# Kernel tuning notes

Hardware: AMD Instinct MI355X
Metric: run time of the kernel (lower is better)

## Reference

```python
import jax, jax.numpy as jnp
import numpy as np

NUM_CAPSULE = 32
DIM_CAPSULE = 16
NUM_ITERATIONS = 3


def squash(v):
    # v: [B, O, F]; squash along last dim
    norm = jnp.linalg.norm(v, axis=-1, keepdims=True)
    mag = norm * norm
    return v / norm * mag / (1.0 + mag)


def setup_inputs() -> dict:
    key = jax.random.key(0)
    k1, k2 = jax.random.split(key)
    B, L, H = 128, 512, 256
    O, F = NUM_CAPSULE, DIM_CAPSULE
    x = jax.random.normal(k1, (B, L, H), dtype=jnp.float32)
    # xavier_normal for [1, H, O*F]: std = sqrt(2 / (H + O*F))
    std = float(np.sqrt(2.0 / (H + O * F)))
    W = jax.random.normal(k2, (1, H, O * F), dtype=jnp.float32) * std
    return {"x": x, "W": W}


def reference(x, W):
    B, I, H = x.shape
    O, F = NUM_CAPSULE, DIM_CAPSULE
    # u: [B, I, O*F] -> [B, O, I, F]
    u = jnp.matmul(x, W)  # broadcasts shared W [1,H,O*F]
    u = u.reshape(B, I, O, F).transpose(0, 2, 1, 3)
    b = jnp.zeros((B, O, I), dtype=u.dtype)
    v = None
    for _ in range(NUM_ITERATIONS):
        c = jax.nn.softmax(b, axis=1)            # softmax over output capsules O
        v = jnp.einsum('boi,boif->bof', c, u)    # weighted aggregation
        v = squash(v)
        b = jnp.einsum('bof,boif->boi', v, u)    # agreement logits
    return v
```

## Files before the change

kernel.cpp:

```cpp
#include <hip/hip_runtime.h>

#define BB 128
#define II 512
#define HH 256
#define OO 32
#define FF 16
#define OF 512
#define CI 64
#define NP 8
#define CSTR 72

typedef __attribute__((ext_vector_type(8))) short short8;
typedef __attribute__((ext_vector_type(4))) float floatx4;

__device__ __forceinline__ ushort f2bf(float f) {
  unsigned u = __float_as_uint(f);
  u += 0x7FFFu + ((u >> 16) & 1u);
  return (ushort)(u >> 16);
}
__device__ __forceinline__ float bf2f(ushort u) {
  return __uint_as_float(((unsigned)u) << 16);
}
__device__ __forceinline__ int swzrow(int i) {
  return (i & 7) ^ (((i >> 3) & 3) << 1);
}

__global__ __launch_bounds__(256) void k_prep(
    const float* __restrict__ x, ushort* __restrict__ x16,
    float* __restrict__ xsum_part) {
  __shared__ float4 red[4][64];
  int t = threadIdx.x;
  int blk = blockIdx.x;
  int c4 = t & 63, grp = t >> 6;
  const float* xg = x + (size_t)blk * CI * HH;
  ushort* x16g = x16 + (size_t)blk * CI * HH;
  int g = c4 >> 1, s4 = (c4 & 1) * 4;
  float4 sum = make_float4(0.f, 0.f, 0.f, 0.f);
#pragma unroll
  for (int j = 0; j < 16; ++j) {
    int row = j * 4 + grp;
    float4 v4 = *(const float4*)(xg + (size_t)row * HH + c4 * 4);
    sum.x += v4.x; sum.y += v4.y; sum.z += v4.z; sum.w += v4.w;
    ushort4 u;
    u.x = f2bf(v4.x); u.y = f2bf(v4.y); u.z = f2bf(v4.z); u.w = f2bf(v4.w);
    *(ushort4*)&x16g[row * HH + (((g ^ swzrow(row)) << 3) + s4)] = u;
  }
  red[grp][c4] = sum;
  __syncthreads();
  if (t < 64) {
    float4 s = red[0][t];
    float4 s1 = red[1][t], s2 = red[2][t], s3 = red[3][t];
    s.x += s1.x + s2.x + s3.x; s.y += s1.y + s2.y + s3.y;
    s.z += s1.z + s2.z + s3.z; s.w += s1.w + s2.w + s3.w;
    *(float4*)&xsum_part[(size_t)blk * HH + t * 4] = s;
  }
}

__global__ __launch_bounds__(256) void k_v1(
    const float* __restrict__ xsum_part, const float* __restrict__ W,
    ushort* __restrict__ wvT16) {
  __shared__ float cxs[HH];
  __shared__ float red[4][16];
  __shared__ float vres[FF];
  int t = threadIdx.x;
  int blk = blockIdx.x;
  int b = blk >> 5, o = blk & 31;
  {
    const float* cp = xsum_part + (size_t)b * NP * HH + t;
    float a = 0.f;
#pragma unroll
    for (int p = 0; p < NP; ++p) a += cp[(size_t)p * HH];
    cxs[t] = a * (1.0f / 32.0f);
  }
  __syncthreads();
  int f = t & 15, hq = t >> 4;
  const float* wp = W + (size_t)hq * 16 * OF + o * FF + f;
  float acc = 0.f;
#pragma unroll
  for (int j = 0; j < 16; ++j)
    acc += cxs[hq * 16 + j] * wp[(size_t)j * OF];
  acc += __shfl_xor(acc, 16);
  acc += __shfl_xor(acc, 32);
  if ((t & 63) < 16) red[t >> 6][f] = acc;
  __syncthreads();
  if (t < 16) {
    float a = red[0][t] + red[1][t] + red[2][t] + red[3][t];
    float n2 = a * a;
#pragma unroll
    for (int mask = 1; mask < 16; mask <<= 1) n2 += __shfl_xor(n2, mask);
    float scale = sqrtf(n2) / (1.f + n2);
    vres[t] = a * scale;
  }
  __syncthreads();
  const float4* wq = (const float4*)(W + (size_t)t * OF + o * FF);
  const float4* vp = (const float4*)vres;
  float a = 0.f;
#pragma unroll
  for (int q = 0; q < 4; ++q) {
    float4 w4 = wq[q], v4 = vp[q];
    a += w4.x * v4.x + w4.y * v4.y + w4.z * v4.z + w4.w * v4.w;
  }
  wvT16[((size_t)b * OO + o) * HH + t] = f2bf(a);
}

__global__ __launch_bounds__(256, 4) void k_route(
    const ushort* __restrict__ x16, const ushort* __restrict__ wvT16,
    ushort* __restrict__ cxp16) {
  __shared__ alignas(16) ushort xs[CI * HH];
  __shared__ alignas(16) ushort c2[OO * CSTR];
  int t = threadIdx.x;
  int blk = blockIdx.x;
  int b = blk >> 3;
  int lane = t & 63, w = t >> 6;
  int l16 = lane & 15, quad = lane >> 4;

  const ushort* gt = x16 + (size_t)blk * (CI * HH);
#pragma unroll
  for (int it = 0; it < 8; ++it) {
    int off = (it * 4 + w) * 512;
    __builtin_amdgcn_global_load_lds(
        (const __attribute__((address_space(1))) unsigned*)(gt + off + lane * 8),
        (__attribute__((address_space(3))) unsigned*)(&xs[off]), 16, 0, 0);
  }
  asm volatile("s_waitcnt vmcnt(0)" ::: "memory");
  __syncthreads();

  int i_a = w * 16 + l16;
  int swa = swzrow(i_a);
  const ushort* xrow = &xs[i_a * HH];
  const ushort* wv0 = wvT16 + ((size_t)b * OO + l16) * HH + quad * 8;
  const ushort* wv1 = wv0 + 16 * HH;
  floatx4 acc0 = {0.f, 0.f, 0.f, 0.f}, acc1 = {0.f, 0.f, 0.f, 0.f};
#pragma unroll
  for (int ks = 0; ks < 8; ++ks) {
    short8 af = *(const short8*)(xrow + (((ks * 4 + quad) ^ swa) << 3));
    short8 b0 = *(const short8*)(wv0 + ks * 32);
    short8 b1 = *(const short8*)(wv1 + ks * 32);
    acc0 = __builtin_amdgcn_mfma_f32_16x16x32_bf16(af, b0, acc0, 0, 0, 0);
    acc1 = __builtin_amdgcn_mfma_f32_16x16x32_bf16(af, b1, acc1, 0, 0, 0);
  }
#pragma unroll
  for (int r = 0; r < 4; ++r) {
    float a0 = acc0[r], a1 = acc1[r];
    float m = fmaxf(a0, a1);
#pragma unroll
    for (int mask = 1; mask < 16; mask <<= 1) m = fmaxf(m, __shfl_xor(m, mask));
    float e0 = __expf(a0 - m), e1 = __expf(a1 - m);
    float s = e0 + e1;
#pragma unroll
    for (int mask = 1; mask < 16; mask <<= 1) s += __shfl_xor(s, mask);
    float inv = 1.f / s;
    int il = w * 16 + quad * 4 + r;
    c2[l16 * CSTR + il] = f2bf(e0 * inv);
    c2[(16 + l16) * CSTR + il] = f2bf(e1 * inv);
  }
  __syncthreads();

  short8 caf[2][2];
#pragma unroll
  for (int mt = 0; mt < 2; ++mt)
#pragma unroll
    for (int ks = 0; ks < 2; ++ks)
      caf[mt][ks] = *(const short8*)&c2[(mt * 16 + l16) * CSTR + ks * 32 + quad * 8];
  ushort* outp0 = cxp16 + (size_t)blk * OO * HH;
#pragma unroll
  for (int hi = 0; hi < 4; ++hi) {
    int ht = w * 4 + hi;
    int hh = ht * 16 + l16;
    int gq = hh >> 3, sub = hh & 7;
    floatx4 d0 = {0.f, 0.f, 0.f, 0.f}, d1 = {0.f, 0.f, 0.f, 0.f};
#pragma unroll
    for (int ks = 0; ks < 2; ++ks) {
      short8 bf;
#pragma unroll
      for (int e = 0; e < 8; ++e) {
        int i = ks * 32 + quad * 8 + e;
        bf[e] = (short)xs[i * HH + (((gq ^ e ^ (quad << 1)) << 3) + sub)];
      }
      d0 = __builtin_amdgcn_mfma_f32_16x16x32_bf16(caf[0][ks], bf, d0, 0, 0, 0);
      d1 = __builtin_amdgcn_mfma_f32_16x16x32_bf16(caf[1][ks], bf, d1, 0, 0, 0);
    }
    ushort* outp = outp0 + ht * 16 + l16;
#pragma unroll
    for (int r = 0; r < 4; ++r) {
      outp[(size_t)(quad * 4 + r) * HH] = f2bf(d0[r]);
      outp[(size_t)(16 + quad * 4 + r) * HH] = f2bf(d1[r]);
    }
  }
}

__global__ __launch_bounds__(256) void k_v2(
    const ushort* __restrict__ cxp16, const float* __restrict__ W,
    ushort* __restrict__ wvT16, float* __restrict__ out, int final_) {
  __shared__ float cxs[HH];
  __shared__ float red[4][16];
  __shared__ float vres[FF];
  int t = threadIdx.x;
  int blk = blockIdx.x;
  int b = blk >> 5, o = blk & 31;
  {
    const ushort* cp = cxp16 + (((size_t)b * NP) * OO + o) * HH + t;
    float a = 0.f;
#pragma unroll
    for (int p = 0; p < NP; ++p) a += bf2f(cp[(size_t)p * OO * HH]);
    cxs[t] = a;
  }
  __syncthreads();
  int f = t & 15, hq = t >> 4;
  const float* wp = W + (size_t)hq * 16 * OF + o * FF + f;
  float acc = 0.f;
#pragma unroll
  for (int j = 0; j < 16; ++j)
    acc += cxs[hq * 16 + j] * wp[(size_t)j * OF];
  acc += __shfl_xor(acc, 16);
  acc += __shfl_xor(acc, 32);
  if ((t & 63) < 16) red[t >> 6][f] = acc;
  __syncthreads();
  if (t < 16) {
    float a = red[0][t] + red[1][t] + red[2][t] + red[3][t];
    float n2 = a * a;
#pragma unroll
    for (int mask = 1; mask < 16; mask <<= 1) n2 += __shfl_xor(n2, mask);
    float scale = sqrtf(n2) / (1.f + n2);
    float res = a * scale;
    if (final_) out[(size_t)blk * FF + t] = res;
    else vres[t] = res;
  }
  if (!final_) {
    __syncthreads();
    const float4* wq = (const float4*)(W + (size_t)t * OF + o * FF);
    const float4* vp = (const float4*)vres;
    float a = 0.f;
#pragma unroll
    for (int q = 0; q < 4; ++q) {
      float4 w4 = wq[q], v4 = vp[q];
      a += w4.x * v4.x + w4.y * v4.y + w4.z * v4.z + w4.w * v4.w;
    }
    wvT16[((size_t)b * OO + o) * HH + t] = f2bf(a);
  }
}

extern "C" void kernel_launch(void* const* d_in, const int* in_sizes, int n_in,
                              void* d_out, int out_size, void* d_ws, size_t ws_size,
                              hipStream_t stream) {
  const float* x = (const float*)d_in[0];
  const float* W = (const float*)d_in[1];
  float* out = (float*)d_out;
  float* ws = (float*)d_ws;
  float*  xsum_part = ws;
  ushort* wvT16 = (ushort*)(ws + 262144);
  ushort* x16   = (ushort*)(ws + 786432);
  ushort* cxp16 = (ushort*)(ws + 9175040);

  k_prep<<<BB * NP, 256, 0, stream>>>(x, x16, xsum_part);
  k_v1<<<BB * OO, 256, 0, stream>>>(xsum_part, W, wvT16);
  for (int it = 0; it < 2; ++it) {
    k_route<<<BB * NP, 256, 0, stream>>>(x16, wvT16, cxp16);
    k_v2<<<BB * OO, 256, 0, stream>>>(cxp16, W, wvT16, out, it == 1);
  }
}
```

Before: 166.8 us.

## Fuse routing iterations into one persistent per-batch kernel

Replaces the separate k_v1, k_route and k_v2 launches with a single 1024-thread kernel, one block per batch. Each block keeps the W·v vectors, the softmax coefficients and the aggregated c·x sums in LDS, and streams x16 in 128-row chunks. This removes four kernel launches and the global round trips through the wvT16 and cxp16 buffers. The cost is a grid of only 128 blocks, which cannot fill all CUs, plus serialized passes with many block-wide barriers and no overlap between chunk loads and compute.

```diff
diff --git a/kernel.cpp b/kernel.cpp
--- a/kernel.cpp
+++ b/kernel.cpp
@@ -8,7 +8,11 @@
 #define OF 512
 #define CI 64
 #define NP 8
-#define CSTR 72
+#define CH 128
+#define NCH 4
+#define WVSTR 264
+#define CSTR2 136
+#define CXSTR 264
 
 typedef __attribute__((ext_vector_type(8))) short short8;
 typedef __attribute__((ext_vector_type(4))) float floatx4;
@@ -48,24 +52,33 @@
   red[grp][c4] = sum;
   __syncthreads();
   if (t < 64) {
-    float4 s = red[0][t];
-    float4 s1 = red[1][t], s2 = red[2][t], s3 = red[3][t];
-    s.x += s1.x + s2.x + s3.x; s.y += s1.y + s2.y + s3.y;
-    s.z += s1.z + s2.z + s3.z; s.w += s1.w + s2.w + s3.w;
-    *(float4*)&xsum_part[(size_t)blk * HH + t * 4] = s;
-  }
-}
-
-__global__ __launch_bounds__(256) void k_v1(
-    const float* __restrict__ xsum_part, const float* __restrict__ W,
-    ushort* __restrict__ wvT16) {
+    float4 s0 = red[0][t], s1 = red[1][t], s2 = red[2][t], s3 = red[3][t];
+    s0.x += s1.x + s2.x + s3.x; s0.y += s1.y + s2.y + s3.y;
+    s0.z += s1.z + s2.z + s3.z; s0.w += s1.w + s2.w + s3.w;
+    *(float4*)&xsum_part[(size_t)blk * HH + t * 4] = s0;
+  }
+}
+
+__global__ __launch_bounds__(1024, 4) void k_main(
+    const ushort* __restrict__ x16, const float* __restrict__ xsum_part,
+    const float* __restrict__ W, float* __restrict__ out) {
+  __shared__ alignas(16) ushort xsc[CH * HH];
+  __shared__ alignas(16) ushort wvs[OO * WVSTR];
+  __shared__ alignas(16) ushort c2[OO * CSTR2];
   __shared__ float cxs[HH];
-  __shared__ float red[4][16];
-  __shared__ float vres[FF];
+  __shared__ float red[4][4][16];
+  __shared__ float vres[4][16];
+  float* cxf = (float*)xsc;
+
   int t = threadIdx.x;
-  int blk = blockIdx.x;
-  int b = blk >> 5, o = blk & 31;
-  {
+  int b = blockIdx.x;
+  int lane = t & 63, w = t >> 6;
+  int l16 = lane & 15, quad = lane >> 4;
+  int g = t >> 8, tg = t & 255;
+  int f = tg & 15, hq = tg >> 4;
+  int wing = tg >> 6;
+
+  if (t < HH) {
     const float* cp = xsum_part + (size_t)b * NP * HH + t;
     float a = 0.f;
 #pragma unroll
@@ -73,170 +86,158 @@
     cxs[t] = a * (1.0f / 32.0f);
   }
   __syncthreads();
-  int f = t & 15, hq = t >> 4;
-  const float* wp = W + (size_t)hq * 16 * OF + o * FF + f;
-  float acc = 0.f;
-#pragma unroll
-  for (int j = 0; j < 16; ++j)
-    acc += cxs[hq * 16 + j] * wp[(size_t)j * OF];
-  acc += __shfl_xor(acc, 16);
-  acc += __shfl_xor(acc, 32);
-  if ((t & 63) < 16) red[t >> 6][f] = acc;
-  __syncthreads();
-  if (t < 16) {
-    float a = red[0][t] + red[1][t] + red[2][t] + red[3][t];
-    float n2 = a * a;
-#pragma unroll
-    for (int mask = 1; mask < 16; mask <<= 1) n2 += __shfl_xor(n2, mask);
-    float scale = sqrtf(n2) / (1.f + n2);
-    vres[t] = a * scale;
-  }
-  __syncthreads();
-  const float4* wq = (const float4*)(W + (size_t)t * OF + o * FF);
-  const float4* vp = (const float4*)vres;
-  float a = 0.f;
-#pragma unroll
-  for (int q = 0; q < 4; ++q) {
-    float4 w4 = wq[q], v4 = vp[q];
-    a += w4.x * v4.x + w4.y * v4.y + w4.z * v4.z + w4.w * v4.w;
-  }
-  wvT16[((size_t)b * OO + o) * HH + t] = f2bf(a);
-}
-
-__global__ __launch_bounds__(256, 4) void k_route(
-    const ushort* __restrict__ x16, const ushort* __restrict__ wvT16,
-    ushort* __restrict__ cxp16) {
-  __shared__ alignas(16) ushort xs[CI * HH];
-  __shared__ alignas(16) ushort c2[OO * CSTR];
-  int t = threadIdx.x;
-  int blk = blockIdx.x;
-  int b = blk >> 3;
-  int lane = t & 63, w = t >> 6;
-  int l16 = lane & 15, quad = lane >> 4;
-
-  const ushort* gt = x16 + (size_t)blk * (CI * HH);
-#pragma unroll
-  for (int it = 0; it < 8; ++it) {
-    int off = (it * 4 + w) * 512;
-    __builtin_amdgcn_global_load_lds(
-        (const __attribute__((address_space(1))) unsigned*)(gt + off + lane * 8),
-        (__attribute__((address_space(3))) unsigned*)(&xs[off]), 16, 0, 0);
-  }
-  asm volatile("s_waitcnt vmcnt(0)" ::: "memory");
-  __syncthreads();
-
-  int i_a = w * 16 + l16;
-  int swa = swzrow(i_a);
-  const ushort* xrow = &xs[i_a * HH];
-  const ushort* wv0 = wvT16 + ((size_t)b * OO + l16) * HH + quad * 8;
-  const ushort* wv1 = wv0 + 16 * HH;
-  floatx4 acc0 = {0.f, 0.f, 0.f, 0.f}, acc1 = {0.f, 0.f, 0.f, 0.f};
-#pragma unroll
-  for (int ks = 0; ks < 8; ++ks) {
-    short8 af = *(const short8*)(xrow + (((ks * 4 + quad) ^ swa) << 3));
-    short8 b0 = *(const short8*)(wv0 + ks * 32);
-    short8 b1 = *(const short8*)(wv1 + ks * 32);
-    acc0 = __builtin_amdgcn_mfma_f32_16x16x32_bf16(af, b0, acc0, 0, 0, 0);
-    acc1 = __builtin_amdgcn_mfma_f32_16x16x32_bf16(af, b1, acc1, 0, 0, 0);
-  }
-#pragma unroll
-  for (int r = 0; r < 4; ++r) {
-    float a0 = acc0[r], a1 = acc1[r];
-    float m = fmaxf(a0, a1);
-#pragma unroll
-    for (int mask = 1; mask < 16; mask <<= 1) m = fmaxf(m, __shfl_xor(m, mask));
-    float e0 = __expf(a0 - m), e1 = __expf(a1 - m);
-    float s = e0 + e1;
-#pragma unroll
-    for (int mask = 1; mask < 16; mask <<= 1) s += __shfl_xor(s, mask);
-    float inv = 1.f / s;
-    int il = w * 16 + quad * 4 + r;
-    c2[l16 * CSTR + il] = f2bf(e0 * inv);
-    c2[(16 + l16) * CSTR + il] = f2bf(e1 * inv);
-  }
-  __syncthreads();
-
-  short8 caf[2][2];
-#pragma unroll
-  for (int mt = 0; mt < 2; ++mt)
-#pragma unroll
-    for (int ks = 0; ks < 2; ++ks)
-      caf[mt][ks] = *(const short8*)&c2[(mt * 16 + l16) * CSTR + ks * 32 + quad * 8];
-  ushort* outp0 = cxp16 + (size_t)blk * OO * HH;
-#pragma unroll
-  for (int hi = 0; hi < 4; ++hi) {
-    int ht = w * 4 + hi;
-    int hh = ht * 16 + l16;
-    int gq = hh >> 3, sub = hh & 7;
+#pragma unroll 1
+  for (int pass = 0; pass < 8; ++pass) {
+    int o = pass * 4 + g;
+    const float* wp = W + (size_t)hq * 16 * OF + o * FF + f;
+    float acc = 0.f;
+#pragma unroll
+    for (int j = 0; j < 16; ++j)
+      acc += cxs[hq * 16 + j] * wp[(size_t)j * OF];
+    acc += __shfl_xor(acc, 16);
+    acc += __shfl_xor(acc, 32);
+    if ((tg & 63) < 16) red[g][wing][f] = acc;
+    __syncthreads();
+    if (tg < 16) {
+      float a2 = red[g][0][tg] + red[g][1][tg] + red[g][2][tg] + red[g][3][tg];
+      float n2 = a2 * a2;
+#pragma unroll
+      for (int mask = 1; mask < 16; mask <<= 1) n2 += __shfl_xor(n2, mask);
+      float scale = sqrtf(n2) / (1.f + n2);
+      vres[g][tg] = a2 * scale;
+    }
+    __syncthreads();
+    {
+      const float4* wq = (const float4*)(W + (size_t)tg * OF + o * FF);
+      const float4* vp = (const float4*)&vres[g][0];
+      float av = 0.f;
+#pragma unroll
+      for (int q = 0; q < 4; ++q) {
+        float4 w4 = wq[q], v4 = vp[q];
+        av += w4.x * v4.x + w4.y * v4.y + w4.z * v4.z + w4.w * v4.w;
+      }
+      wvs[o * WVSTR + tg] = f2bf(av);
+    }
+    __syncthreads();
+  }
+
+#pragma unroll 1
+  for (int it = 0; it < 2; ++it) {
     floatx4 d0 = {0.f, 0.f, 0.f, 0.f}, d1 = {0.f, 0.f, 0.f, 0.f};
-#pragma unroll
-    for (int ks = 0; ks < 2; ++ks) {
-      short8 bf;
-#pragma unroll
-      for (int e = 0; e < 8; ++e) {
-        int i = ks * 32 + quad * 8 + e;
-        bf[e] = (short)xs[i * HH + (((gq ^ e ^ (quad << 1)) << 3) + sub)];
-      }
-      d0 = __builtin_amdgcn_mfma_f32_16x16x32_bf16(caf[0][ks], bf, d0, 0, 0, 0);
-      d1 = __builtin_amdgcn_mfma_f32_16x16x32_bf16(caf[1][ks], bf, d1, 0, 0, 0);
-    }
-    ushort* outp = outp0 + ht * 16 + l16;
-#pragma unroll
-    for (int r = 0; r < 4; ++r) {
-      outp[(size_t)(quad * 4 + r) * HH] = f2bf(d0[r]);
-      outp[(size_t)(16 + quad * 4 + r) * HH] = f2bf(d1[r]);
-    }
-  }
-}
-
-__global__ __launch_bounds__(256) void k_v2(
-    const ushort* __restrict__ cxp16, const float* __restrict__ W,
-    ushort* __restrict__ wvT16, float* __restrict__ out, int final_) {
-  __shared__ float cxs[HH];
-  __shared__ float red[4][16];
-  __shared__ float vres[FF];
-  int t = threadIdx.x;
-  int blk = blockIdx.x;
-  int b = blk >> 5, o = blk & 31;
-  {
-    const ushort* cp = cxp16 + (((size_t)b * NP) * OO + o) * HH + t;
-    float a = 0.f;
-#pragma unroll
-    for (int p = 0; p < NP; ++p) a += bf2f(cp[(size_t)p * OO * HH]);
-    cxs[t] = a;
-  }
-  __syncthreads();
-  int f = t & 15, hq = t >> 4;
-  const float* wp = W + (size_t)hq * 16 * OF + o * FF + f;
-  float acc = 0.f;
-#pragma unroll
-  for (int j = 0; j < 16; ++j)
-    acc += cxs[hq * 16 + j] * wp[(size_t)j * OF];
-  acc += __shfl_xor(acc, 16);
-  acc += __shfl_xor(acc, 32);
-  if ((t & 63) < 16) red[t >> 6][f] = acc;
-  __syncthreads();
-  if (t < 16) {
-    float a = red[0][t] + red[1][t] + red[2][t] + red[3][t];
-    float n2 = a * a;
-#pragma unroll
-    for (int mask = 1; mask < 16; mask <<= 1) n2 += __shfl_xor(n2, mask);
-    float scale = sqrtf(n2) / (1.f + n2);
-    float res = a * scale;
-    if (final_) out[(size_t)blk * FF + t] = res;
-    else vres[t] = res;
-  }
-  if (!final_) {
-    __syncthreads();
-    const float4* wq = (const float4*)(W + (size_t)t * OF + o * FF);
-    const float4* vp = (const float4*)vres;
-    float a = 0.f;
-#pragma unroll
-    for (int q = 0; q < 4; ++q) {
-      float4 w4 = wq[q], v4 = vp[q];
-      a += w4.x * v4.x + w4.y * v4.y + w4.z * v4.z + w4.w * v4.w;
-    }
-    wvT16[((size_t)b * OO + o) * HH + t] = f2bf(a);
+#pragma unroll 1
+    for (int ch = 0; ch < NCH; ++ch) {
+      const ushort* gt = x16 + ((size_t)b * NP + ch * 2) * CI * HH;
+#pragma unroll
+      for (int s = 0; s < 4; ++s) {
+        int off = (s * 16 + w) * 512;
+        __builtin_amdgcn_global_load_lds(
+            (const __attribute__((address_space(1))) unsigned*)(gt + off + lane * 8),
+            (__attribute__((address_space(3))) unsigned*)(&xsc[off]), 16, 0, 0);
+      }
+      asm volatile("s_waitcnt vmcnt(0)" ::: "memory");
+      __syncthreads();
+
+      if (w < 8) {
+        int i_l = w * 16 + l16;
+        int swa = swzrow(i_l);
+        const ushort* xrow = &xsc[i_l * HH];
+        const ushort* wv0 = &wvs[l16 * WVSTR + quad * 8];
+        const ushort* wv1 = wv0 + 16 * WVSTR;
+        floatx4 a0 = {0.f, 0.f, 0.f, 0.f}, a1 = {0.f, 0.f, 0.f, 0.f};
+#pragma unroll
+        for (int ks = 0; ks < 8; ++ks) {
+          short8 af = *(const short8*)(xrow + (((ks * 4 + quad) ^ swa) << 3));
+          short8 b0 = *(const short8*)(wv0 + ks * 32);
+          short8 b1 = *(const short8*)(wv1 + ks * 32);
+          a0 = __builtin_amdgcn_mfma_f32_16x16x32_bf16(af, b0, a0, 0, 0, 0);
+          a1 = __builtin_amdgcn_mfma_f32_16x16x32_bf16(af, b1, a1, 0, 0, 0);
+        }
+#pragma unroll
+        for (int r = 0; r < 4; ++r) {
+          float v0 = a0[r], v1 = a1[r];
+          float m = fmaxf(v0, v1);
+#pragma unroll
+          for (int mask = 1; mask < 16; mask <<= 1) m = fmaxf(m, __shfl_xor(m, mask));
+          float e0 = __expf(v0 - m), e1 = __expf(v1 - m);
+          float s = e0 + e1;
+#pragma unroll
+          for (int mask = 1; mask < 16; mask <<= 1) s += __shfl_xor(s, mask);
+          float inv = 1.f / s;
+          int il = w * 16 + quad * 4 + r;
+          c2[l16 * CSTR2 + il] = f2bf(e0 * inv);
+          c2[(16 + l16) * CSTR2 + il] = f2bf(e1 * inv);
+        }
+      }
+      __syncthreads();
+
+      {
+        int hh = w * 16 + l16;
+        int gq = hh >> 3, sub = hh & 7;
+#pragma unroll
+        for (int ks = 0; ks < 4; ++ks) {
+          short8 caf0 = *(const short8*)&c2[l16 * CSTR2 + ks * 32 + quad * 8];
+          short8 caf1 = *(const short8*)&c2[(16 + l16) * CSTR2 + ks * 32 + quad * 8];
+          short8 bf;
+#pragma unroll
+          for (int e = 0; e < 8; ++e) {
+            int i = ks * 32 + quad * 8 + e;
+            bf[e] = (short)xsc[i * HH + (((gq ^ e ^ (quad << 1)) << 3) + sub)];
+          }
+          d0 = __builtin_amdgcn_mfma_f32_16x16x32_bf16(caf0, bf, d0, 0, 0, 0);
+          d1 = __builtin_amdgcn_mfma_f32_16x16x32_bf16(caf1, bf, d1, 0, 0, 0);
+        }
+      }
+      __syncthreads();
+    }
+
+    {
+      int hcol = w * 16 + l16;
+#pragma unroll
+      for (int r = 0; r < 4; ++r) {
+        cxf[(quad * 4 + r) * CXSTR + hcol] = d0[r];
+        cxf[(16 + quad * 4 + r) * CXSTR + hcol] = d1[r];
+      }
+    }
+    __syncthreads();
+
+    int final_ = (it == 1);
+#pragma unroll 1
+    for (int pass = 0; pass < 8; ++pass) {
+      int o = pass * 4 + g;
+      const float* crow = &cxf[o * CXSTR];
+      const float* wp = W + (size_t)hq * 16 * OF + o * FF + f;
+      float acc = 0.f;
+#pragma unroll
+      for (int j = 0; j < 16; ++j)
+        acc += crow[hq * 16 + j] * wp[(size_t)j * OF];
+      acc += __shfl_xor(acc, 16);
+      acc += __shfl_xor(acc, 32);
+      if ((tg & 63) < 16) red[g][wing][f] = acc;
+      __syncthreads();
+      if (tg < 16) {
+        float a2 = red[g][0][tg] + red[g][1][tg] + red[g][2][tg] + red[g][3][tg];
+        float n2 = a2 * a2;
+#pragma unroll
+        for (int mask = 1; mask < 16; mask <<= 1) n2 += __shfl_xor(n2, mask);
+        float scale = sqrtf(n2) / (1.f + n2);
+        float res = a2 * scale;
+        if (final_) out[((size_t)b * OO + o) * FF + tg] = res;
+        else vres[g][tg] = res;
+      }
+      __syncthreads();
+      if (!final_) {
+        const float4* wq = (const float4*)(W + (size_t)tg * OF + o * FF);
+        const float4* vp = (const float4*)&vres[g][0];
+        float av = 0.f;
+#pragma unroll
+        for (int q = 0; q < 4; ++q) {
+          float4 w4 = wq[q], v4 = vp[q];
+          av += w4.x * v4.x + w4.y * v4.y + w4.z * v4.z + w4.w * v4.w;
+        }
+        wvs[o * WVSTR + tg] = f2bf(av);
+      }
+      __syncthreads();
+    }
   }
 }
 
@@ -248,14 +249,8 @@
   float* out = (float*)d_out;
   float* ws = (float*)d_ws;
   float*  xsum_part = ws;
-  ushort* wvT16 = (ushort*)(ws + 262144);
-  ushort* x16   = (ushort*)(ws + 786432);
-  ushort* cxp16 = (ushort*)(ws + 9175040);
+  ushort* x16 = (ushort*)(ws + 262144);
 
   k_prep<<<BB * NP, 256, 0, stream>>>(x, x16, xsum_part);
-  k_v1<<<BB * OO, 256, 0, stream>>>(xsum_part, W, wvT16);
-  for (int it = 0; it < 2; ++it) {
-    k_route<<<BB * NP, 256, 0, stream>>>(x16, wvT16, cxp16);
-    k_v2<<<BB * OO, 256, 0, stream>>>(cxp16, W, wvT16, out, it == 1);
-  }
-}
+  k_main<<<BB, 1024, 0, stream>>>(x16, xsum_part, W, out);
+}
```

Result: slower. 200.1 us (+19.9%).
